# Optimization experiments

Measured on AMD Instinct MI355X. Metric: run time of the kernel, lower is better.

Reference implementation:

```python
import jax, jax.numpy as jnp
import numpy as np
import math

B, L, D, H = 4, 2048, 768, 6
HD = D // H  # head_dim = 128

def setup_inputs() -> dict:
    key = jax.random.key(0)
    ks = jax.random.split(key, 9)
    s = 0.02
    return {
        "x": jax.random.normal(ks[0], (B, L, D), dtype=jnp.float32),
        "Wq": jax.random.normal(ks[1], (D, D), dtype=jnp.float32) * s,
        "bq": jnp.zeros((D,), dtype=jnp.float32),
        "Wk": jax.random.normal(ks[2], (D, D), dtype=jnp.float32) * s,
        "bk": jnp.zeros((D,), dtype=jnp.float32),
        "Wv": jax.random.normal(ks[3], (D, D), dtype=jnp.float32) * s,
        "bv": jnp.zeros((D,), dtype=jnp.float32),
        "Wo": jax.random.normal(ks[4], (D, D), dtype=jnp.float32) * s,
        "bo": jnp.zeros((D,), dtype=jnp.float32),
    }

def _split_heads(t):
    # [b, l, h*d] -> [b, h, l, d]
    b, l, _ = t.shape
    return t.reshape(b, l, H, HD).transpose(0, 2, 1, 3)

def reference(x, Wq, bq, Wk, bk, Wv, bv, Wo, bo):
    q = _split_heads(x @ Wq + bq)
    k = _split_heads(x @ Wk + bk)
    v = _split_heads(x @ Wv + bv)
    scores = jnp.einsum("bhqd,bhkd->bhqk", q, k) / math.sqrt(HD)
    # Original builds jnp.tril(ones, k=1) and fills mask==0 positions; it
    # mistakenly used +inf there, which yields NaN — we use -inf (intended
    # masking math) while keeping the same tril(k=1) pattern.
    l = x.shape[1]
    mask = jnp.tril(jnp.ones((l, l), dtype=bool), k=1)
    logits = jnp.where(mask, scores, -jnp.inf)
    attn = jax.nn.softmax(logits, axis=-1)
    out = jnp.einsum("bhqk,bhkd->bhqd", attn, v)
    out = out.transpose(0, 2, 1, 3).reshape(x.shape[0], l, D)
    # dropout in eval/deterministic mode: identity
    return out @ Wo + bo
```

## Files before the change

kernel.cpp:

```cpp
#include <hip/hip_runtime.h>
#include <math.h>

#define HEADS 6
#define SEQ   2048
#define DIM   768
#define HDIM  128
#define BATCH 4
#define MTOT  (BATCH*SEQ)
#define NKV   (SEQ/32)
#define NCHUNK_TOT 83

typedef float  f32x4   __attribute__((ext_vector_type(4)));
typedef __bf16 bf16x8  __attribute__((ext_vector_type(8)));
typedef __bf16 bf16x4  __attribute__((ext_vector_type(4)));
typedef float  f32x4v  __attribute__((ext_vector_type(4)));

typedef __attribute__((address_space(3))) void lds_v;
typedef __attribute__((address_space(1))) void gbl_v;

__device__ __forceinline__ f32x4 mfma16(bf16x8 a, bf16x8 b, f32x4 c) {
    return __builtin_amdgcn_mfma_f32_16x16x32_bf16(a, b, c, 0, 0, 0);
}
__device__ __forceinline__ unsigned int bperm(int srclane, unsigned int v) {
    return (unsigned int)__builtin_amdgcn_ds_bpermute(srclane << 2, (int)v);
}
__device__ __forceinline__ unsigned int cvtpk(float lo, float hi) {
    unsigned int r;
    asm("v_cvt_pk_bf16_f32 %0, %1, %2" : "=v"(r) : "v"(lo), "v"(hi));
    return r;
}

__global__ __launch_bounds__(256) void prep_kernel(
    const float* __restrict__ x, __bf16* __restrict__ xb,
    const float* __restrict__ W0, const float* __restrict__ W1,
    const float* __restrict__ W2, const float* __restrict__ W3,
    __bf16* __restrict__ T0, __bf16* __restrict__ T1,
    __bf16* __restrict__ T2, __bf16* __restrict__ T3) {
    __shared__ float tile[32][33];
    if (blockIdx.x < 6144) {
        int i = (blockIdx.x * 256 + threadIdx.x) * 4;
        f32x4v v = *(const f32x4v*)(x + i);
        bf16x4 o;
        o[0] = (__bf16)v[0]; o[1] = (__bf16)v[1];
        o[2] = (__bf16)v[2]; o[3] = (__bf16)v[3];
        *(bf16x4*)(xb + i) = o;
        return;
    }
    const int bid = blockIdx.x - 6144;
    const int z = bid / 576, r = bid % 576;
    const int bx = r % 24, by = r / 24;
    const float* W; __bf16* T;
    if      (z == 0) { W = W0; T = T0; }
    else if (z == 1) { W = W1; T = T1; }
    else if (z == 2) { W = W2; T = T2; }
    else             { W = W3; T = T3; }
    int n0 = bx * 32, k0 = by * 32;
    int tx = threadIdx.x & 31, ty = threadIdx.x >> 5;
#pragma unroll
    for (int i = 0; i < 4; ++i)
        tile[ty + i*8][tx] = W[(size_t)(k0 + ty + i*8) * DIM + n0 + tx];
    __syncthreads();
#pragma unroll
    for (int i = 0; i < 4; ++i)
        T[(size_t)(n0 + ty + i*8) * DIM + k0 + tx] = (__bf16)tile[tx][ty + i*8];
}

#define GEMM_PIPE(A_PTR, B_PTR, NKSTEP)                                           \
    __shared__ __align__(16) __bf16 As[3][128 * 32];                              \
    __shared__ __align__(16) __bf16 Bs[3][128 * 32];                              \
    const int tid  = threadIdx.x;                                                 \
    const int wave = tid >> 6, lane = tid & 63;                                   \
    const int l16  = lane & 15, lh = lane >> 4;                                   \
    const int wr = wave >> 1, wc = wave & 1;                                      \
    f32x4 acc[4][4] = {};                                                         \
    auto stage = [&](int buf, int step) {                                         \
        const int k0 = step * 32;                                                 \
        _Pragma("unroll")                                                         \
        for (int ci = 0; ci < 4; ++ci) {                                          \
            int c = wave * 4 + ci;                                                \
            int t = c & 7;                                                        \
            int e = (t * 64 + lane) * 8;                                          \
            int r = e >> 5, kk = e & 31;                                          \
            const __bf16* gp = (c < 8) ? ((A_PTR) + (size_t)(m0 + r) * DIM + k0 + kk) \
                                       : ((B_PTR) + (size_t)(n0 + r) * DIM + k0 + kk); \
            __bf16* lp = (c < 8 ? As[buf] : Bs[buf]) + t * 512;                   \
            __builtin_amdgcn_global_load_lds((const gbl_v*)gp, (lds_v*)lp, 16, 0, 0); \
        }                                                                         \
    };                                                                            \
    stage(0, 0); stage(1, 1);                                                     \
    asm volatile("s_waitcnt vmcnt(4)" ::: "memory");                              \
    __builtin_amdgcn_s_barrier();                                                 \
    for (int t = 0; t < (NKSTEP); ++t) {                                          \
        const int cur = t % 3;                                                    \
        if (t + 2 < (NKSTEP)) stage((t + 2) % 3, t + 2);                          \
        bf16x8 af[4], bfr[4];                                                     \
        _Pragma("unroll")                                                         \
        for (int i = 0; i < 4; ++i)                                               \
            af[i] = *(const bf16x8*)&As[cur][(wr*64 + i*16 + l16) * 32 + lh*8];   \
        _Pragma("unroll")                                                         \
        for (int j = 0; j < 4; ++j)                                               \
            bfr[j] = *(const bf16x8*)&Bs[cur][(wc*64 + j*16 + l16) * 32 + lh*8];  \
        __builtin_amdgcn_s_setprio(1);                                            \
        _Pragma("unroll")                                                         \
        for (int i = 0; i < 4; ++i)                                               \
            _Pragma("unroll")                                                     \
            for (int j = 0; j < 4; ++j)                                           \
                acc[i][j] = mfma16(af[i], bfr[j], acc[i][j]);                     \
        __builtin_amdgcn_s_setprio(0);                                            \
        if (t + 2 < (NKSTEP))      asm volatile("s_waitcnt vmcnt(4)" ::: "memory"); \
        else if (t + 1 < (NKSTEP)) asm volatile("s_waitcnt vmcnt(0)" ::: "memory"); \
        __builtin_amdgcn_s_barrier();                                             \
    }

__global__ __launch_bounds__(256) void gemm_qkv(const __bf16* __restrict__ A,
                                                const __bf16* __restrict__ Wcat,
                                                const float* __restrict__ bq,
                                                const float* __restrict__ bk,
                                                const float* __restrict__ bv,
                                                __bf16* __restrict__ Qb,
                                                __bf16* __restrict__ Kb,
                                                __bf16* __restrict__ Vt) {
    constexpr int NWG = (MTOT/128) * (2304/128);
    const int swz = (blockIdx.x & 7) * (NWG >> 3) + (blockIdx.x >> 3);
    const int bn = swz % (2304 / 128), bm = swz / (2304 / 128);
    const int m0 = bm * 128, n0 = bn * 128;
    GEMM_PIPE(A, Wcat, 24)

    const int sel = n0 / DIM;
    const float* bias = sel == 0 ? bq : (sel == 1 ? bk : bv);
#pragma unroll
    for (int i = 0; i < 4; ++i) {
        int row = m0 + wr*64 + i*16 + lh*4;
#pragma unroll
        for (int j = 0; j < 4; ++j) {
            int col  = n0 + wc*64 + j*16 + l16;
            int lcol = col - sel * DIM;
            float bvv = bias[lcol];
            if (sel < 2) {
                __bf16* o = (sel == 0) ? Qb : Kb;
#pragma unroll
                for (int r = 0; r < 4; ++r)
                    o[(size_t)(row + r) * DIM + lcol] = (__bf16)(acc[i][j][r] + bvv);
            } else {
                int bb = row >> 11, ll = row & (SEQ - 1);
                int hh = lcol >> 7, dd = lcol & (HDIM - 1);
                bf16x4 pk;
#pragma unroll
                for (int r = 0; r < 4; ++r) pk[r] = (__bf16)(acc[i][j][r] + bvv);
                *(bf16x4*)&Vt[((size_t)((bb*HEADS + hh) * HDIM + dd)) * SEQ + ll] = pk;
            }
        }
    }
}

__global__ __launch_bounds__(256) void gemm_out(const __bf16* __restrict__ A,
                                                const __bf16* __restrict__ Bt,
                                                const float* __restrict__ bias,
                                                float* __restrict__ outp) {
    constexpr int NWG = (MTOT/128) * (DIM/128);
    const int swz = (blockIdx.x & 7) * (NWG >> 3) + (blockIdx.x >> 3);
    const int bn = swz % (DIM / 128), bm = swz / (DIM / 128);
    const int m0 = bm * 128, n0 = bn * 128;
    GEMM_PIPE(A, Bt, 24)

#pragma unroll
    for (int i = 0; i < 4; ++i) {
        int row = m0 + wr*64 + i*16 + lh*4;
#pragma unroll
        for (int j = 0; j < 4; ++j) {
            int col = n0 + wc*64 + j*16 + l16;
            float bv = bias[col];
#pragma unroll
            for (int r = 0; r < 4; ++r)
                outp[(size_t)(row + r) * DIM + col] = acc[i][j][r] + bv;
        }
    }
}

__global__ __launch_bounds__(256, 3) void attn_kernel(
    const __bf16* __restrict__ Q, const __bf16* __restrict__ K,
    const __bf16* __restrict__ Vt,
    __bf16* __restrict__ po, float* __restrict__ pm, float* __restrict__ pl,
    __bf16* __restrict__ Ob) {
    __shared__ __align__(16) __bf16 Ks[2][32 * 128];
    __shared__ __align__(16) __bf16 Vs[2][128 * 32];
    const int lane = threadIdx.x & 63, wv = threadIdx.x >> 6;
    const int l16 = lane & 15, lh = lane >> 4;
    const int id  = blockIdx.x;
    const int xcd = id & 7;
    const int idx = id >> 3;
    const int bh_l = idx % 3;
    const int ci = (NCHUNK_TOT - 1) - idx / 3;
    int tile, chunk;
    if      (ci < 7)  { tile = ci;                chunk = 0;          }
    else if (ci < 23) { tile = 7  + (ci-7)/2;     chunk = (ci-7)&1;   }
    else if (ci < 47) { tile = 15 + (ci-23)/3;    chunk = (ci-23)%3;  }
    else              { tile = 23 + (ci-47)/4;    chunk = (ci-47)&3;  }
    const int cstart = ci - chunk;
    const int bh = xcd + 8 * bh_l;
    const int b = bh / HEADS, h = bh - b * HEADS;
    const int qw0 = tile * 64 + wv * 16;
    const int nkb = min(2 * tile + 3, NKV);
    const int nc  = (nkb + 15) >> 4;
    const int lo  = chunk * 16;
    const int cnt = min(lo + 16, nkb) - lo;
    const float qs = 0.12751674770951932f;

    bf16x8 qf[4];
    {
        const __bf16* qp = Q + (size_t)(b*SEQ + qw0 + l16) * DIM + h*HDIM + lh*8;
#pragma unroll
        for (int kk = 0; kk < 4; ++kk) {
            bf16x8 v = *(const bf16x8*)(qp + kk*32);
            bf16x8 sv;
#pragma unroll
            for (int e = 0; e < 8; ++e) sv[e] = (__bf16)((float)v[e] * qs);
            qf[kk] = sv;
        }
    }

    const __bf16* kgb = K  + (size_t)(b*SEQ) * DIM + h*HDIM;
    const __bf16* vgb = Vt + (size_t)bh * HDIM * SEQ;

    auto stage = [&](int buf, int kb) {
        const int kbase = kb * 32;
#pragma unroll
        for (int s = 0; s < 4; ++s) {
            const int j = wv * 4 + s;
            if (j < 8) {
                const int row = j * 4 + (lane >> 4);
                const int c16 = (lane & 15) ^ (row & 7);
                const __bf16* gp = kgb + (size_t)(kbase + row) * DIM + c16 * 8;
                __builtin_amdgcn_global_load_lds((const gbl_v*)gp,
                    (lds_v*)&Ks[buf][j * 512], 16, 0, 0);
            } else {
                const int jj = j - 8;
                const int row = jj * 16 + (lane >> 2);
                const int c16 = (lane & 3) ^ ((row >> 1) & 3);
                const __bf16* gp = vgb + (size_t)row * SEQ + kbase + c16 * 8;
                __builtin_amdgcn_global_load_lds((const gbl_v*)gp,
                    (lds_v*)&Vs[buf][jj * 512], 16, 0, 0);
            }
        }
    };

    f32x4 o[8] = {};
    float mx = -INFINITY, lsum = 0.f;

    stage(0, lo);
    asm volatile("s_waitcnt vmcnt(0)" ::: "memory");
    __builtin_amdgcn_s_barrier();

    int cur = 0;
    for (int i = 0; i < cnt; ++i) {
        const int kb = lo + i;
        const int kbase = kb * 32;
        const bool more = (i + 1 < cnt);
        if (more) {
            stage(cur ^ 1, kb + 1);
            asm volatile("s_waitcnt vmcnt(4)" ::: "memory");
        } else {
            asm volatile("s_waitcnt vmcnt(0)" ::: "memory");
        }
        __builtin_amdgcn_s_barrier();

        if (kbase <= qw0 + 16) {
            bf16x8 kfA[4], kfB[4];
#pragma unroll
            for (int kk = 0; kk < 4; ++kk) {
                const int ca = (kk*4 + lh) ^ (l16 & 7);
                kfA[kk] = *(const bf16x8*)&Ks[cur][l16 * 128 + ca * 8];
                const int rb = 16 + l16;
                const int cb = (kk*4 + lh) ^ (rb & 7);
                kfB[kk] = *(const bf16x8*)&Ks[cur][rb * 128 + cb * 8];
            }
            f32x4 sA = {}, sB = {};
            __builtin_amdgcn_s_setprio(1);
#pragma unroll
            for (int kk = 0; kk < 4; ++kk) {
                sA = mfma16(kfA[kk], qf[kk], sA);
                sB = mfma16(kfB[kk], qf[kk], sB);
            }
            __builtin_amdgcn_s_setprio(0);
            const int q = qw0 + l16;
            float p[8];
#pragma unroll
            for (int r = 0; r < 4; ++r) { p[r] = sA[r]; p[r+4] = sB[r]; }
            if (kbase + 30 > qw0) {
#pragma unroll
                for (int r = 0; r < 4; ++r) {
                    const int key = kbase + lh*4 + r;
                    if (key      > q + 1) p[r]   = -INFINITY;
                    if (key + 16 > q + 1) p[r+4] = -INFINITY;
                }
            }
            float m0 = p[0];
#pragma unroll
            for (int t2 = 1; t2 < 8; ++t2) m0 = fmaxf(m0, p[t2]);
            m0 = fmaxf(m0, __shfl_xor(m0, 16));
            m0 = fmaxf(m0, __shfl_xor(m0, 32));
            const bool defer = __all(m0 <= mx + 8.f && mx > -3e38f);
            if (!defer) {
                const float mnew = fmaxf(mx, m0);
                const float resc = (mx < mnew) ? exp2f(mx - mnew) : 1.0f;
                lsum *= resc;
#pragma unroll
                for (int d = 0; d < 8; ++d)
#pragma unroll
                    for (int r = 0; r < 4; ++r) o[d][r] *= resc;
                mx = mnew;
            }
            const float mref = (mx == -INFINITY) ? 0.f : mx;
#pragma unroll
            for (int t2 = 0; t2 < 8; ++t2) p[t2] = exp2f(p[t2] - mref);
            float rs = 0.f;
#pragma unroll
            for (int t2 = 0; t2 < 8; ++t2) rs += p[t2];
            rs += __shfl_xor(rs, 16);
            rs += __shfl_xor(rs, 32);
            lsum += rs;
            unsigned int w0 = cvtpk(p[0], p[1]);
            unsigned int w1 = cvtpk(p[2], p[3]);
            unsigned int w2 = cvtpk(p[4], p[5]);
            unsigned int w3 = cvtpk(p[6], p[7]);
            const int s0l = l16 + ((lh & 1) << 5);
            unsigned int A0 = bperm(s0l,      w0), A1 = bperm(s0l,      w1);
            unsigned int A2 = bperm(s0l,      w2), A3 = bperm(s0l,      w3);
            unsigned int B0 = bperm(s0l + 16, w0), B1 = bperm(s0l + 16, w1);
            unsigned int B2 = bperm(s0l + 16, w2), B3 = bperm(s0l + 16, w3);
            const bool hi = (lh >= 2);
            union { unsigned int u[4]; bf16x8 v; } pu;
            pu.u[0] = hi ? A2 : A0;
            pu.u[1] = hi ? A3 : A1;
            pu.u[2] = hi ? B2 : B0;
            pu.u[3] = hi ? B3 : B1;
            const bf16x8 pf = pu.v;
            __builtin_amdgcn_s_setprio(1);
#pragma unroll
            for (int d = 0; d < 8; ++d) {
                const int row = d * 16 + l16;
                const int cv = lh ^ ((row >> 1) & 3);
                bf16x8 vf = *(const bf16x8*)&Vs[cur][row * 32 + cv * 8];
                o[d] = mfma16(vf, pf, o[d]);
            }
            __builtin_amdgcn_s_setprio(0);
        }
        __builtin_amdgcn_s_barrier();
        cur ^= 1;
    }

    if (nc == 1) {
        const float inv = 1.0f / lsum;
        __bf16* op = Ob + (size_t)(b*SEQ + qw0 + l16) * DIM + h*HDIM;
#pragma unroll
        for (int d = 0; d < 8; ++d) {
            bf16x4 pk;
#pragma unroll
            for (int r = 0; r < 4; ++r) pk[r] = (__bf16)(o[d][r] * inv);
            *(bf16x4*)(op + d*16 + lh*4) = pk;
        }
    } else {
        const int pid = bh * NCHUNK_TOT + cstart + chunk;
        const int lq  = wv * 16 + l16;
        __bf16* pop = po + ((size_t)pid * 64 + lq) * HDIM;
#pragma unroll
        for (int d = 0; d < 8; ++d) {
            bf16x4 pk;
#pragma unroll
            for (int r = 0; r < 4; ++r) pk[r] = (__bf16)o[d][r];
            *(bf16x4*)(pop + d*16 + lh*4) = pk;
        }
        if (lh == 0) {
            pm[(size_t)pid * 64 + lq] = mx;
            pl[(size_t)pid * 64 + lq] = lsum;
        }
    }
}

__global__ __launch_bounds__(256) void merge_kernel(const __bf16* __restrict__ po,
    const float* __restrict__ pm, const float* __restrict__ pl,
    __bf16* __restrict__ Ob) {
    const int id = blockIdx.x;
    const int bh = id / 25;
    const int tile = 7 + id % 25;
    int cstart, nc;
    if      (tile < 15) { cstart = 7  + (tile-7)*2;   nc = 2; }
    else if (tile < 23) { cstart = 23 + (tile-15)*3;  nc = 3; }
    else                { cstart = 47 + (tile-23)*4;  nc = 4; }
    const int b = bh / HEADS, h = bh - b * HEADS;
    const int lq = threadIdx.x >> 2;
    const int d0 = (threadIdx.x & 3) * 32;
    const size_t pb = (size_t)bh * NCHUNK_TOT + cstart;
    float M = -INFINITY;
    for (int cc = 0; cc < nc; ++cc) M = fmaxf(M, pm[(pb + cc) * 64 + lq]);
    float L = 0.f, w[4] = {0.f, 0.f, 0.f, 0.f};
    for (int cc = 0; cc < nc; ++cc) {
        w[cc] = exp2f(pm[(pb + cc) * 64 + lq] - M);
        L += w[cc] * pl[(pb + cc) * 64 + lq];
    }
    const float invL = 1.0f / L;
    __bf16* op = Ob + (size_t)(b*SEQ + tile*64 + lq) * DIM + h*HDIM;
#pragma unroll
    for (int d = 0; d < 32; d += 8) {
        float acc[8] = {};
        for (int cc = 0; cc < nc; ++cc) {
            bf16x8 v = *(const bf16x8*)&po[((pb + cc) * 64 + lq) * HDIM + d0 + d];
            const float wc = w[cc];
#pragma unroll
            for (int e = 0; e < 8; ++e) acc[e] += wc * (float)v[e];
        }
        bf16x8 ov;
#pragma unroll
        for (int e = 0; e < 8; ++e) ov[e] = (__bf16)(acc[e] * invL);
        *(bf16x8*)(op + d0 + d) = ov;
    }
}

extern "C" void kernel_launch(void* const* d_in, const int* in_sizes, int n_in,
                              void* d_out, int out_size, void* d_ws, size_t ws_size,
                              hipStream_t stream) {
    const float* x  = (const float*)d_in[0];
    const float* Wq = (const float*)d_in[1];
    const float* bq = (const float*)d_in[2];
    const float* Wk = (const float*)d_in[3];
    const float* bk = (const float*)d_in[4];
    const float* Wv = (const float*)d_in[5];
    const float* bv = (const float*)d_in[6];
    const float* Wo = (const float*)d_in[7];
    const float* bo = (const float*)d_in[8];

    char* p = (char*)d_ws;
    const size_t SZ_X = (size_t)MTOT * DIM * 2;
    const size_t SZ_W = (size_t)DIM * DIM * 2;
    __bf16* xb   = (__bf16*)p; p += SZ_X;
    __bf16* Wcat = (__bf16*)p; p += 3 * SZ_W;
    __bf16* Wto  = (__bf16*)p; p += SZ_W;
    __bf16* Qb   = (__bf16*)p; p += SZ_X;
    __bf16* Kb   = (__bf16*)p; p += SZ_X;
    __bf16* Vt   = (__bf16*)p; p += SZ_X;
    __bf16* Ob   = xb;

    const size_t SZ_PO = (size_t)24 * NCHUNK_TOT * 64 * HDIM * 2;
    const size_t SZ_PM = (size_t)24 * NCHUNK_TOT * 64 * 4;
    __bf16* po  = (__bf16*)p;           p += SZ_PO;
    float*  pmv = (float*)p;            p += SZ_PM;
    float*  plv = (float*)p;

    prep_kernel<<<6144 + 2304, 256, 0, stream>>>(
        x, xb, Wq, Wk, Wv, Wo,
        Wcat, Wcat + (size_t)DIM*DIM, Wcat + (size_t)2*DIM*DIM, Wto);

    gemm_qkv<<<(MTOT/128) * (2304/128), 256, 0, stream>>>(xb, Wcat, bq, bk, bv, Qb, Kb, Vt);

    attn_kernel<<<8 * 3 * NCHUNK_TOT, 256, 0, stream>>>(Qb, Kb, Vt, po, pmv, plv, Ob);
    merge_kernel<<<24 * 25, 256, 0, stream>>>(po, pmv, plv, Ob);

    gemm_out<<<(MTOT/128) * (DIM/128), 256, 0, stream>>>(Ob, Wto, bo, (float*)d_out);
}
```

Baseline: 163.7 us.

## Make attention kernel persistent with per-XCD atomic work queues

Replaces the static one-block-per-chunk grid with a persistent grid of 1280 blocks. Each block reads its XCC_ID hardware register and pulls work items from a per-XCD atomic counter, keeping each XCD on its own heads, processing the largest chunks first. The counters are zeroed in prep_kernel. This is meant to balance the causal-triangle work across CUs and cut tail imbalance, at the cost of an atomic plus two block barriers per item and reliance on the hardware XCC id for the head mapping.

```diff
diff --git a/kernel.cpp b/kernel.cpp
--- a/kernel.cpp
+++ b/kernel.cpp
@@ -9,6 +9,7 @@
 #define MTOT  (BATCH*SEQ)
 #define NKV   (SEQ/32)
 #define NCHUNK_TOT 83
+#define QPX   (3 * NCHUNK_TOT)
 
 typedef float  f32x4   __attribute__((ext_vector_type(4)));
 typedef __bf16 bf16x8  __attribute__((ext_vector_type(8)));
@@ -35,8 +36,10 @@
     const float* __restrict__ W0, const float* __restrict__ W1,
     const float* __restrict__ W2, const float* __restrict__ W3,
     __bf16* __restrict__ T0, __bf16* __restrict__ T1,
-    __bf16* __restrict__ T2, __bf16* __restrict__ T3) {
+    __bf16* __restrict__ T2, __bf16* __restrict__ T3,
+    unsigned int* __restrict__ qcnt) {
     __shared__ float tile[32][33];
+    if (blockIdx.x == 0 && threadIdx.x < 8) qcnt[threadIdx.x] = 0;
     if (blockIdx.x < 6144) {
         int i = (blockIdx.x * 256 + threadIdx.x) * 4;
         f32x4v v = *(const f32x4v*)(x + i);
@@ -181,198 +184,208 @@
     const __bf16* __restrict__ Q, const __bf16* __restrict__ K,
     const __bf16* __restrict__ Vt,
     __bf16* __restrict__ po, float* __restrict__ pm, float* __restrict__ pl,
-    __bf16* __restrict__ Ob) {
+    __bf16* __restrict__ Ob, unsigned int* __restrict__ qcnt) {
     __shared__ __align__(16) __bf16 Ks[2][32 * 128];
     __shared__ __align__(16) __bf16 Vs[2][128 * 32];
     const int lane = threadIdx.x & 63, wv = threadIdx.x >> 6;
     const int l16 = lane & 15, lh = lane >> 4;
-    const int id  = blockIdx.x;
-    const int xcd = id & 7;
-    const int idx = id >> 3;
-    const int bh_l = idx % 3;
-    const int ci = (NCHUNK_TOT - 1) - idx / 3;
-    int tile, chunk;
-    if      (ci < 7)  { tile = ci;                chunk = 0;          }
-    else if (ci < 23) { tile = 7  + (ci-7)/2;     chunk = (ci-7)&1;   }
-    else if (ci < 47) { tile = 15 + (ci-23)/3;    chunk = (ci-23)%3;  }
-    else              { tile = 23 + (ci-47)/4;    chunk = (ci-47)&3;  }
-    const int cstart = ci - chunk;
-    const int bh = xcd + 8 * bh_l;
-    const int b = bh / HEADS, h = bh - b * HEADS;
-    const int qw0 = tile * 64 + wv * 16;
-    const int nkb = min(2 * tile + 3, NKV);
-    const int nc  = (nkb + 15) >> 4;
-    const int lo  = chunk * 16;
-    const int cnt = min(lo + 16, nkb) - lo;
+    unsigned int xcc;
+    asm volatile("s_getreg_b32 %0, hwreg(HW_REG_XCC_ID)" : "=s"(xcc));
+    const int xcd = (int)(xcc & 7);
     const float qs = 0.12751674770951932f;
 
-    bf16x8 qf[4];
-    {
-        const __bf16* qp = Q + (size_t)(b*SEQ + qw0 + l16) * DIM + h*HDIM + lh*8;
-#pragma unroll
-        for (int kk = 0; kk < 4; ++kk) {
-            bf16x8 v = *(const bf16x8*)(qp + kk*32);
-            bf16x8 sv;
-#pragma unroll
-            for (int e = 0; e < 8; ++e) sv[e] = (__bf16)((float)v[e] * qs);
-            qf[kk] = sv;
-        }
-    }
-
-    const __bf16* kgb = K  + (size_t)(b*SEQ) * DIM + h*HDIM;
-    const __bf16* vgb = Vt + (size_t)bh * HDIM * SEQ;
-
-    auto stage = [&](int buf, int kb) {
-        const int kbase = kb * 32;
-#pragma unroll
-        for (int s = 0; s < 4; ++s) {
-            const int j = wv * 4 + s;
-            if (j < 8) {
-                const int row = j * 4 + (lane >> 4);
-                const int c16 = (lane & 15) ^ (row & 7);
-                const __bf16* gp = kgb + (size_t)(kbase + row) * DIM + c16 * 8;
-                __builtin_amdgcn_global_load_lds((const gbl_v*)gp,
-                    (lds_v*)&Ks[buf][j * 512], 16, 0, 0);
+    for (;;) {
+        if (threadIdx.x == 0)
+            *(volatile int*)&Ks[0][0] = (int)atomicAdd(&qcnt[xcd], 1u);
+        __syncthreads();
+        const int pos = *(volatile int*)&Ks[0][0];
+        __syncthreads();
+        if (pos >= QPX) break;
+
+        const int bh_l = pos % 3;
+        const int ci = (NCHUNK_TOT - 1) - pos / 3;
+        int tile, chunk;
+        if      (ci < 7)  { tile = ci;                chunk = 0;          }
+        else if (ci < 23) { tile = 7  + (ci-7)/2;     chunk = (ci-7)&1;   }
+        else if (ci < 47) { tile = 15 + (ci-23)/3;    chunk = (ci-23)%3;  }
+        else              { tile = 23 + (ci-47)/4;    chunk = (ci-47)&3;  }
+        const int cstart = ci - chunk;
+        const int bh = xcd + 8 * bh_l;
+        const int b = bh / HEADS, h = bh - b * HEADS;
+        const int qw0 = tile * 64 + wv * 16;
+        const int nkb = min(2 * tile + 3, NKV);
+        const int nc  = (nkb + 15) >> 4;
+        const int lo  = chunk * 16;
+        const int cnt = min(lo + 16, nkb) - lo;
+
+        bf16x8 qf[4];
+        {
+            const __bf16* qp = Q + (size_t)(b*SEQ + qw0 + l16) * DIM + h*HDIM + lh*8;
+#pragma unroll
+            for (int kk = 0; kk < 4; ++kk) {
+                bf16x8 v = *(const bf16x8*)(qp + kk*32);
+                bf16x8 sv;
+#pragma unroll
+                for (int e = 0; e < 8; ++e) sv[e] = (__bf16)((float)v[e] * qs);
+                qf[kk] = sv;
+            }
+        }
+
+        const __bf16* kgb = K  + (size_t)(b*SEQ) * DIM + h*HDIM;
+        const __bf16* vgb = Vt + (size_t)bh * HDIM * SEQ;
+
+        auto stage = [&](int buf, int kb) {
+            const int kbase = kb * 32;
+#pragma unroll
+            for (int s = 0; s < 4; ++s) {
+                const int j = wv * 4 + s;
+                if (j < 8) {
+                    const int row = j * 4 + (lane >> 4);
+                    const int c16 = (lane & 15) ^ (row & 7);
+                    const __bf16* gp = kgb + (size_t)(kbase + row) * DIM + c16 * 8;
+                    __builtin_amdgcn_global_load_lds((const gbl_v*)gp,
+                        (lds_v*)&Ks[buf][j * 512], 16, 0, 0);
+                } else {
+                    const int jj = j - 8;
+                    const int row = jj * 16 + (lane >> 2);
+                    const int c16 = (lane & 3) ^ ((row >> 1) & 3);
+                    const __bf16* gp = vgb + (size_t)row * SEQ + kbase + c16 * 8;
+                    __builtin_amdgcn_global_load_lds((const gbl_v*)gp,
+                        (lds_v*)&Vs[buf][jj * 512], 16, 0, 0);
+                }
+            }
+        };
+
+        f32x4 o[8] = {};
+        float mx = -INFINITY, lsum = 0.f;
+
+        stage(0, lo);
+        asm volatile("s_waitcnt vmcnt(0)" ::: "memory");
+        __builtin_amdgcn_s_barrier();
+
+        int cur = 0;
+        for (int i = 0; i < cnt; ++i) {
+            const int kb = lo + i;
+            const int kbase = kb * 32;
+            const bool more = (i + 1 < cnt);
+            if (more) {
+                stage(cur ^ 1, kb + 1);
+                asm volatile("s_waitcnt vmcnt(4)" ::: "memory");
             } else {
-                const int jj = j - 8;
-                const int row = jj * 16 + (lane >> 2);
-                const int c16 = (lane & 3) ^ ((row >> 1) & 3);
-                const __bf16* gp = vgb + (size_t)row * SEQ + kbase + c16 * 8;
-                __builtin_amdgcn_global_load_lds((const gbl_v*)gp,
-                    (lds_v*)&Vs[buf][jj * 512], 16, 0, 0);
-            }
-        }
-    };
-
-    f32x4 o[8] = {};
-    float mx = -INFINITY, lsum = 0.f;
-
-    stage(0, lo);
-    asm volatile("s_waitcnt vmcnt(0)" ::: "memory");
-    __builtin_amdgcn_s_barrier();
-
-    int cur = 0;
-    for (int i = 0; i < cnt; ++i) {
-        const int kb = lo + i;
-        const int kbase = kb * 32;
-        const bool more = (i + 1 < cnt);
-        if (more) {
-            stage(cur ^ 1, kb + 1);
-            asm volatile("s_waitcnt vmcnt(4)" ::: "memory");
+                asm volatile("s_waitcnt vmcnt(0)" ::: "memory");
+            }
+            __builtin_amdgcn_s_barrier();
+
+            if (kbase <= qw0 + 16) {
+                bf16x8 kfA[4], kfB[4];
+#pragma unroll
+                for (int kk = 0; kk < 4; ++kk) {
+                    const int ca = (kk*4 + lh) ^ (l16 & 7);
+                    kfA[kk] = *(const bf16x8*)&Ks[cur][l16 * 128 + ca * 8];
+                    const int rb = 16 + l16;
+                    const int cb = (kk*4 + lh) ^ (rb & 7);
+                    kfB[kk] = *(const bf16x8*)&Ks[cur][rb * 128 + cb * 8];
+                }
+                f32x4 sA = {}, sB = {};
+                __builtin_amdgcn_s_setprio(1);
+#pragma unroll
+                for (int kk = 0; kk < 4; ++kk) {
+                    sA = mfma16(kfA[kk], qf[kk], sA);
+                    sB = mfma16(kfB[kk], qf[kk], sB);
+                }
+                __builtin_amdgcn_s_setprio(0);
+                const int q = qw0 + l16;
+                float p[8];
+#pragma unroll
+                for (int r = 0; r < 4; ++r) { p[r] = sA[r]; p[r+4] = sB[r]; }
+                if (kbase + 30 > qw0) {
+#pragma unroll
+                    for (int r = 0; r < 4; ++r) {
+                        const int key = kbase + lh*4 + r;
+                        if (key      > q + 1) p[r]   = -INFINITY;
+                        if (key + 16 > q + 1) p[r+4] = -INFINITY;
+                    }
+                }
+                float m0 = p[0];
+#pragma unroll
+                for (int t2 = 1; t2 < 8; ++t2) m0 = fmaxf(m0, p[t2]);
+                m0 = fmaxf(m0, __shfl_xor(m0, 16));
+                m0 = fmaxf(m0, __shfl_xor(m0, 32));
+                const bool defer = __all(m0 <= mx + 8.f && mx > -3e38f);
+                if (!defer) {
+                    const float mnew = fmaxf(mx, m0);
+                    const float resc = (mx < mnew) ? exp2f(mx - mnew) : 1.0f;
+                    lsum *= resc;
+#pragma unroll
+                    for (int d = 0; d < 8; ++d)
+#pragma unroll
+                        for (int r = 0; r < 4; ++r) o[d][r] *= resc;
+                    mx = mnew;
+                }
+                const float mref = (mx == -INFINITY) ? 0.f : mx;
+#pragma unroll
+                for (int t2 = 0; t2 < 8; ++t2) p[t2] = exp2f(p[t2] - mref);
+                float rs = 0.f;
+#pragma unroll
+                for (int t2 = 0; t2 < 8; ++t2) rs += p[t2];
+                rs += __shfl_xor(rs, 16);
+                rs += __shfl_xor(rs, 32);
+                lsum += rs;
+                unsigned int w0 = cvtpk(p[0], p[1]);
+                unsigned int w1 = cvtpk(p[2], p[3]);
+                unsigned int w2 = cvtpk(p[4], p[5]);
+                unsigned int w3 = cvtpk(p[6], p[7]);
+                const int s0l = l16 + ((lh & 1) << 5);
+                unsigned int A0 = bperm(s0l,      w0), A1 = bperm(s0l,      w1);
+                unsigned int A2 = bperm(s0l,      w2), A3 = bperm(s0l,      w3);
+                unsigned int B0 = bperm(s0l + 16, w0), B1 = bperm(s0l + 16, w1);
+                unsigned int B2 = bperm(s0l + 16, w2), B3 = bperm(s0l + 16, w3);
+                const bool hi = (lh >= 2);
+                union { unsigned int u[4]; bf16x8 v; } pu;
+                pu.u[0] = hi ? A2 : A0;
+                pu.u[1] = hi ? A3 : A1;
+                pu.u[2] = hi ? B2 : B0;
+                pu.u[3] = hi ? B3 : B1;
+                const bf16x8 pf = pu.v;
+                __builtin_amdgcn_s_setprio(1);
+#pragma unroll
+                for (int d = 0; d < 8; ++d) {
+                    const int row = d * 16 + l16;
+                    const int cv = lh ^ ((row >> 1) & 3);
+                    bf16x8 vf = *(const bf16x8*)&Vs[cur][row * 32 + cv * 8];
+                    o[d] = mfma16(vf, pf, o[d]);
+                }
+                __builtin_amdgcn_s_setprio(0);
+            }
+            __builtin_amdgcn_s_barrier();
+            cur ^= 1;
+        }
+
+        if (nc == 1) {
+            const float inv = 1.0f / lsum;
+            __bf16* op = Ob + (size_t)(b*SEQ + qw0 + l16) * DIM + h*HDIM;
+#pragma unroll
+            for (int d = 0; d < 8; ++d) {
+                bf16x4 pk;
+#pragma unroll
+                for (int r = 0; r < 4; ++r) pk[r] = (__bf16)(o[d][r] * inv);
+                *(bf16x4*)(op + d*16 + lh*4) = pk;
+            }
         } else {
-            asm volatile("s_waitcnt vmcnt(0)" ::: "memory");
-        }
-        __builtin_amdgcn_s_barrier();
-
-        if (kbase <= qw0 + 16) {
-            bf16x8 kfA[4], kfB[4];
-#pragma unroll
-            for (int kk = 0; kk < 4; ++kk) {
-                const int ca = (kk*4 + lh) ^ (l16 & 7);
-                kfA[kk] = *(const bf16x8*)&Ks[cur][l16 * 128 + ca * 8];
-                const int rb = 16 + l16;
-                const int cb = (kk*4 + lh) ^ (rb & 7);
-                kfB[kk] = *(const bf16x8*)&Ks[cur][rb * 128 + cb * 8];
-            }
-            f32x4 sA = {}, sB = {};
-            __builtin_amdgcn_s_setprio(1);
-#pragma unroll
-            for (int kk = 0; kk < 4; ++kk) {
-                sA = mfma16(kfA[kk], qf[kk], sA);
-                sB = mfma16(kfB[kk], qf[kk], sB);
-            }
-            __builtin_amdgcn_s_setprio(0);
-            const int q = qw0 + l16;
-            float p[8];
-#pragma unroll
-            for (int r = 0; r < 4; ++r) { p[r] = sA[r]; p[r+4] = sB[r]; }
-            if (kbase + 30 > qw0) {
-#pragma unroll
-                for (int r = 0; r < 4; ++r) {
-                    const int key = kbase + lh*4 + r;
-                    if (key      > q + 1) p[r]   = -INFINITY;
-                    if (key + 16 > q + 1) p[r+4] = -INFINITY;
-                }
-            }
-            float m0 = p[0];
-#pragma unroll
-            for (int t2 = 1; t2 < 8; ++t2) m0 = fmaxf(m0, p[t2]);
-            m0 = fmaxf(m0, __shfl_xor(m0, 16));
-            m0 = fmaxf(m0, __shfl_xor(m0, 32));
-            const bool defer = __all(m0 <= mx + 8.f && mx > -3e38f);
-            if (!defer) {
-                const float mnew = fmaxf(mx, m0);
-                const float resc = (mx < mnew) ? exp2f(mx - mnew) : 1.0f;
-                lsum *= resc;
-#pragma unroll
-                for (int d = 0; d < 8; ++d)
-#pragma unroll
-                    for (int r = 0; r < 4; ++r) o[d][r] *= resc;
-                mx = mnew;
-            }
-            const float mref = (mx == -INFINITY) ? 0.f : mx;
-#pragma unroll
-            for (int t2 = 0; t2 < 8; ++t2) p[t2] = exp2f(p[t2] - mref);
-            float rs = 0.f;
-#pragma unroll
-            for (int t2 = 0; t2 < 8; ++t2) rs += p[t2];
-            rs += __shfl_xor(rs, 16);
-            rs += __shfl_xor(rs, 32);
-            lsum += rs;
-            unsigned int w0 = cvtpk(p[0], p[1]);
-            unsigned int w1 = cvtpk(p[2], p[3]);
-            unsigned int w2 = cvtpk(p[4], p[5]);
-            unsigned int w3 = cvtpk(p[6], p[7]);
-            const int s0l = l16 + ((lh & 1) << 5);
-            unsigned int A0 = bperm(s0l,      w0), A1 = bperm(s0l,      w1);
-            unsigned int A2 = bperm(s0l,      w2), A3 = bperm(s0l,      w3);
-            unsigned int B0 = bperm(s0l + 16, w0), B1 = bperm(s0l + 16, w1);
-            unsigned int B2 = bperm(s0l + 16, w2), B3 = bperm(s0l + 16, w3);
-            const bool hi = (lh >= 2);
-            union { unsigned int u[4]; bf16x8 v; } pu;
-            pu.u[0] = hi ? A2 : A0;
-            pu.u[1] = hi ? A3 : A1;
-            pu.u[2] = hi ? B2 : B0;
-            pu.u[3] = hi ? B3 : B1;
-            const bf16x8 pf = pu.v;
-            __builtin_amdgcn_s_setprio(1);
+            const int pid = bh * NCHUNK_TOT + cstart + chunk;
+            const int lq  = wv * 16 + l16;
+            __bf16* pop = po + ((size_t)pid * 64 + lq) * HDIM;
 #pragma unroll
             for (int d = 0; d < 8; ++d) {
-                const int row = d * 16 + l16;
-                const int cv = lh ^ ((row >> 1) & 3);
-                bf16x8 vf = *(const bf16x8*)&Vs[cur][row * 32 + cv * 8];
-                o[d] = mfma16(vf, pf, o[d]);
-            }
-            __builtin_amdgcn_s_setprio(0);
-        }
-        __builtin_amdgcn_s_barrier();
-        cur ^= 1;
-    }
-
-    if (nc == 1) {
-        const float inv = 1.0f / lsum;
-        __bf16* op = Ob + (size_t)(b*SEQ + qw0 + l16) * DIM + h*HDIM;
-#pragma unroll
-        for (int d = 0; d < 8; ++d) {
-            bf16x4 pk;
-#pragma unroll
-            for (int r = 0; r < 4; ++r) pk[r] = (__bf16)(o[d][r] * inv);
-            *(bf16x4*)(op + d*16 + lh*4) = pk;
-        }
-    } else {
-        const int pid = bh * NCHUNK_TOT + cstart + chunk;
-        const int lq  = wv * 16 + l16;
-        __bf16* pop = po + ((size_t)pid * 64 + lq) * HDIM;
-#pragma unroll
-        for (int d = 0; d < 8; ++d) {
-            bf16x4 pk;
-#pragma unroll
-            for (int r = 0; r < 4; ++r) pk[r] = (__bf16)o[d][r];
-            *(bf16x4*)(pop + d*16 + lh*4) = pk;
-        }
-        if (lh == 0) {
-            pm[(size_t)pid * 64 + lq] = mx;
-            pl[(size_t)pid * 64 + lq] = lsum;
+                bf16x4 pk;
+#pragma unroll
+                for (int r = 0; r < 4; ++r) pk[r] = (__bf16)o[d][r];
+                *(bf16x4*)(pop + d*16 + lh*4) = pk;
+            }
+            if (lh == 0) {
+                pm[(size_t)pid * 64 + lq] = mx;
+                pl[(size_t)pid * 64 + lq] = lsum;
+            }
         }
     }
 }
@@ -444,15 +457,16 @@
     const size_t SZ_PM = (size_t)24 * NCHUNK_TOT * 64 * 4;
     __bf16* po  = (__bf16*)p;           p += SZ_PO;
     float*  pmv = (float*)p;            p += SZ_PM;
-    float*  plv = (float*)p;
+    float*  plv = (float*)p;            p += SZ_PM;
+    unsigned int* qcnt = (unsigned int*)p;
 
     prep_kernel<<<6144 + 2304, 256, 0, stream>>>(
         x, xb, Wq, Wk, Wv, Wo,
-        Wcat, Wcat + (size_t)DIM*DIM, Wcat + (size_t)2*DIM*DIM, Wto);
+        Wcat, Wcat + (size_t)DIM*DIM, Wcat + (size_t)2*DIM*DIM, Wto, qcnt);
 
     gemm_qkv<<<(MTOT/128) * (2304/128), 256, 0, stream>>>(xb, Wcat, bq, bk, bv, Qb, Kb, Vt);
 
-    attn_kernel<<<8 * 3 * NCHUNK_TOT, 256, 0, stream>>>(Qb, Kb, Vt, po, pmv, plv, Ob);
+    attn_kernel<<<1280, 256, 0, stream>>>(Qb, Kb, Vt, po, pmv, plv, Ob, qcnt);
     merge_kernel<<<24 * 25, 256, 0, stream>>>(po, pmv, plv, Ob);
 
     gemm_out<<<(MTOT/128) * (DIM/128), 256, 0, stream>>>(Ob, Wto, bo, (float*)d_out);
```

After: 171.8 us. 1.05x slower.

## Fuse split-KV merge into attention kernel via last-arriver atomic counter

Applied to the files above, without the earlier changes.

Removes the separate merge kernel launch. Each split chunk block of the attention kernel writes its partial output, fences, and atomically increments a per-(head, tile) counter that the prep kernel zeroes. The last-arriving block then merges the partials into the final output. This saves one launch and the gap between kernels, at the cost of a fence, an atomic and a tail merge done by a single block, which relies on correct memory ordering.

```diff
diff --git a/kernel.cpp b/kernel.cpp
--- a/kernel.cpp
+++ b/kernel.cpp
@@ -35,8 +35,11 @@
     const float* __restrict__ W0, const float* __restrict__ W1,
     const float* __restrict__ W2, const float* __restrict__ W3,
     __bf16* __restrict__ T0, __bf16* __restrict__ T1,
-    __bf16* __restrict__ T2, __bf16* __restrict__ T3) {
+    __bf16* __restrict__ T2, __bf16* __restrict__ T3,
+    unsigned int* __restrict__ tcnt) {
     __shared__ float tile[32][33];
+    if (blockIdx.x == 0)
+        for (int i = threadIdx.x; i < 24 * 32; i += 256) tcnt[i] = 0;
     if (blockIdx.x < 6144) {
         int i = (blockIdx.x * 256 + threadIdx.x) * 4;
         f32x4v v = *(const f32x4v*)(x + i);
@@ -181,7 +184,7 @@
     const __bf16* __restrict__ Q, const __bf16* __restrict__ K,
     const __bf16* __restrict__ Vt,
     __bf16* __restrict__ po, float* __restrict__ pm, float* __restrict__ pl,
-    __bf16* __restrict__ Ob) {
+    __bf16* __restrict__ Ob, unsigned int* __restrict__ tcnt) {
     __shared__ __align__(16) __bf16 Ks[2][32 * 128];
     __shared__ __align__(16) __bf16 Vs[2][128 * 32];
     const int lane = threadIdx.x & 63, wv = threadIdx.x >> 6;
@@ -359,9 +362,13 @@
             for (int r = 0; r < 4; ++r) pk[r] = (__bf16)(o[d][r] * inv);
             *(bf16x4*)(op + d*16 + lh*4) = pk;
         }
-    } else {
-        const int pid = bh * NCHUNK_TOT + cstart + chunk;
-        const int lq  = wv * 16 + l16;
+        return;
+    }
+
+    {
+        const size_t pb  = (size_t)bh * NCHUNK_TOT + cstart;
+        const int   pid  = (int)pb + chunk;
+        const int   lq   = wv * 16 + l16;
         __bf16* pop = po + ((size_t)pid * 64 + lq) * HDIM;
 #pragma unroll
         for (int d = 0; d < 8; ++d) {
@@ -374,45 +381,40 @@
             pm[(size_t)pid * 64 + lq] = mx;
             pl[(size_t)pid * 64 + lq] = lsum;
         }
-    }
-}
-
-__global__ __launch_bounds__(256) void merge_kernel(const __bf16* __restrict__ po,
-    const float* __restrict__ pm, const float* __restrict__ pl,
-    __bf16* __restrict__ Ob) {
-    const int id = blockIdx.x;
-    const int bh = id / 25;
-    const int tile = 7 + id % 25;
-    int cstart, nc;
-    if      (tile < 15) { cstart = 7  + (tile-7)*2;   nc = 2; }
-    else if (tile < 23) { cstart = 23 + (tile-15)*3;  nc = 3; }
-    else                { cstart = 47 + (tile-23)*4;  nc = 4; }
-    const int b = bh / HEADS, h = bh - b * HEADS;
-    const int lq = threadIdx.x >> 2;
-    const int d0 = (threadIdx.x & 3) * 32;
-    const size_t pb = (size_t)bh * NCHUNK_TOT + cstart;
-    float M = -INFINITY;
-    for (int cc = 0; cc < nc; ++cc) M = fmaxf(M, pm[(pb + cc) * 64 + lq]);
-    float L = 0.f, w[4] = {0.f, 0.f, 0.f, 0.f};
-    for (int cc = 0; cc < nc; ++cc) {
-        w[cc] = exp2f(pm[(pb + cc) * 64 + lq] - M);
-        L += w[cc] * pl[(pb + cc) * 64 + lq];
-    }
-    const float invL = 1.0f / L;
-    __bf16* op = Ob + (size_t)(b*SEQ + tile*64 + lq) * DIM + h*HDIM;
-#pragma unroll
-    for (int d = 0; d < 32; d += 8) {
-        float acc[8] = {};
+        __threadfence();
+        __syncthreads();
+        if (threadIdx.x == 0)
+            *(volatile unsigned int*)&Ks[0][0] =
+                atomicAdd(&tcnt[bh * 32 + tile], 1u);
+        __syncthreads();
+        const unsigned int tk = *(volatile unsigned int*)&Ks[0][0];
+        if (tk != (unsigned int)(nc - 1)) return;
+
+        const int lq2 = threadIdx.x >> 2;
+        const int d02 = (threadIdx.x & 3) * 32;
+        float M = -INFINITY;
+        for (int cc = 0; cc < nc; ++cc) M = fmaxf(M, pm[(pb + cc) * 64 + lq2]);
+        float L = 0.f, w[4] = {0.f, 0.f, 0.f, 0.f};
         for (int cc = 0; cc < nc; ++cc) {
-            bf16x8 v = *(const bf16x8*)&po[((pb + cc) * 64 + lq) * HDIM + d0 + d];
-            const float wc = w[cc];
-#pragma unroll
-            for (int e = 0; e < 8; ++e) acc[e] += wc * (float)v[e];
-        }
-        bf16x8 ov;
-#pragma unroll
-        for (int e = 0; e < 8; ++e) ov[e] = (__bf16)(acc[e] * invL);
-        *(bf16x8*)(op + d0 + d) = ov;
+            w[cc] = exp2f(pm[(pb + cc) * 64 + lq2] - M);
+            L += w[cc] * pl[(pb + cc) * 64 + lq2];
+        }
+        const float invL = 1.0f / L;
+        __bf16* op = Ob + (size_t)(b*SEQ + tile*64 + lq2) * DIM + h*HDIM;
+#pragma unroll
+        for (int d = 0; d < 32; d += 8) {
+            float acc[8] = {};
+            for (int cc = 0; cc < nc; ++cc) {
+                bf16x8 v = *(const bf16x8*)&po[((pb + cc) * 64 + lq2) * HDIM + d02 + d];
+                const float wc = w[cc];
+#pragma unroll
+                for (int e = 0; e < 8; ++e) acc[e] += wc * (float)v[e];
+            }
+            bf16x8 ov;
+#pragma unroll
+            for (int e = 0; e < 8; ++e) ov[e] = (__bf16)(acc[e] * invL);
+            *(bf16x8*)(op + d02 + d) = ov;
+        }
     }
 }
 
@@ -444,16 +446,16 @@
     const size_t SZ_PM = (size_t)24 * NCHUNK_TOT * 64 * 4;
     __bf16* po  = (__bf16*)p;           p += SZ_PO;
     float*  pmv = (float*)p;            p += SZ_PM;
-    float*  plv = (float*)p;
+    float*  plv = (float*)p;            p += SZ_PM;
+    unsigned int* tcnt = (unsigned int*)p;
 
     prep_kernel<<<6144 + 2304, 256, 0, stream>>>(
         x, xb, Wq, Wk, Wv, Wo,
-        Wcat, Wcat + (size_t)DIM*DIM, Wcat + (size_t)2*DIM*DIM, Wto);
+        Wcat, Wcat + (size_t)DIM*DIM, Wcat + (size_t)2*DIM*DIM, Wto, tcnt);
 
     gemm_qkv<<<(MTOT/128) * (2304/128), 256, 0, stream>>>(xb, Wcat, bq, bk, bv, Qb, Kb, Vt);
 
-    attn_kernel<<<8 * 3 * NCHUNK_TOT, 256, 0, stream>>>(Qb, Kb, Vt, po, pmv, plv, Ob);
-    merge_kernel<<<24 * 25, 256, 0, stream>>>(po, pmv, plv, Ob);
+    attn_kernel<<<8 * 3 * NCHUNK_TOT, 256, 0, stream>>>(Qb, Kb, Vt, po, pmv, plv, Ob, tcnt);
 
     gemm_out<<<(MTOT/128) * (DIM/128), 256, 0, stream>>>(Ob, Wto, bo, (float*)d_out);
 }
```

Result: slower. 393.9 us (+140.6%).
